# Kernel tuning notes

Hardware: AMD Instinct MI355X
Metric: run time of the kernel (lower is better)

The kernel has to match this reference:

```python
import jax, jax.numpy as jnp
from jax import lax
import numpy as np

H, W, C = 128, 128, 1024          # backbone feature map (stride-16, ResNet C4)
STRIDE = 16
NUM_ANCHORS = 9                   # 3 scales x 3 ratios
IOU_THRESHOLD = 0.7
SCORE_THRESHOLD = 0.5


def _make_anchors():
    scales = np.array([128.0, 256.0, 512.0], np.float32)
    ratios = np.array([0.5, 1.0, 2.0], np.float32)
    hs = (scales[:, None] * np.sqrt(ratios)[None, :]).reshape(-1)   # [9]
    ws = (scales[:, None] / np.sqrt(ratios)[None, :]).reshape(-1)   # [9]
    cy = (np.arange(H, dtype=np.float32) + 0.5) * STRIDE
    cx = (np.arange(W, dtype=np.float32) + 0.5) * STRIDE
    anc = np.zeros((H, W, NUM_ANCHORS, 4), np.float32)
    anc[..., 0] = cy[:, None, None]
    anc[..., 1] = cx[None, :, None]
    anc[..., 2] = hs
    anc[..., 3] = ws
    return anc.reshape(-1, 4)      # [N,4] as (cy, cx, h, w)


def _conv(x, w, b):
    return lax.conv_general_dilated(
        x, w, (1, 1), 'SAME', dimension_numbers=('NHWC', 'HWIO', 'NHWC')) + b


def _rpn_head(features, w1, b1, w2, b2, w_score, b_score, w_box, b_box):
    x = jax.nn.relu(features)
    x = _conv(x, w1, b1)
    x = jax.nn.relu(x)
    x = _conv(x, w2, b2)
    scores = jax.nn.sigmoid(_conv(x, w_score, b_score))   # [1,H,W,9]
    shifts = _conv(x, w_box, b_box)                        # [1,H,W,36]
    return scores.reshape(-1, 1), shifts.reshape(-1, 4)


def _decode(shifts, anchors):
    acy, acx, ah, aw = anchors[:, 0], anchors[:, 1], anchors[:, 2], anchors[:, 3]
    dy, dx, dh, dw = shifts[:, 0], shifts[:, 1], shifts[:, 2], shifts[:, 3]
    cy = acy + dy * ah
    cx = acx + dx * aw
    h = ah * jnp.exp(dh)
    w = aw * jnp.exp(dw)
    y1 = jnp.clip(cy - 0.5 * h, 0.0, H * STRIDE)
    x1 = jnp.clip(cx - 0.5 * w, 0.0, W * STRIDE)
    y2 = jnp.clip(cy + 0.5 * h, 0.0, H * STRIDE)
    x2 = jnp.clip(cx + 0.5 * w, 0.0, W * STRIDE)
    return jnp.stack([y1, x1, y2, x2], axis=-1)            # [N,4]


def _nms(boxes, scores, max_out):
    """Greedy NMS like tf.image.non_max_suppression, fixed-size padded output."""
    n = boxes.shape[0]
    areas = (boxes[:, 2] - boxes[:, 0]) * (boxes[:, 3] - boxes[:, 1])

    def body(state):
        suppressed, sel, count = state
        masked = jnp.where(suppressed, -jnp.inf, scores)
        i = jnp.argmax(masked)
        valid = masked[i] >= SCORE_THRESHOLD
        sel = sel.at[count].set(jnp.where(valid, i.astype(jnp.int32), -1))
        count = count + valid.astype(jnp.int32)
        b = boxes[i]
        iy = jnp.maximum(0.0, jnp.minimum(b[2], boxes[:, 2]) - jnp.maximum(b[0], boxes[:, 0]))
        ix = jnp.maximum(0.0, jnp.minimum(b[3], boxes[:, 3]) - jnp.maximum(b[1], boxes[:, 1]))
        inter = iy * ix
        iou = inter / (areas[i] + areas - inter + 1e-9)
        new_sup = (suppressed | (iou > IOU_THRESHOLD)).at[i].set(True)
        suppressed = jnp.where(valid, new_sup, jnp.ones_like(suppressed))
        return suppressed, sel, count

    def cond(state):
        suppressed, sel, count = state
        return (count < max_out) & (~jnp.all(suppressed))

    sel0 = jnp.full((max_out,), -1, jnp.int32)
    sup0 = jnp.zeros((n,), bool)
    _, sel, _ = lax.while_loop(cond, body, (sup0, sel0, jnp.int32(0)))
    valid = sel >= 0
    idx = jnp.where(valid, sel, 0)
    return boxes[idx] * valid[:, None], scores[idx] * valid, valid


def setup_inputs() -> dict:
    key = jax.random.key(0)
    ks = jax.random.split(key, 5)
    def init_w(k, shape, fan_in, scale=1.0):
        return jax.random.normal(k, shape, jnp.float32) * (scale / np.sqrt(fan_in))
    features = jax.random.normal(ks[0], (1, H, W, C), jnp.float32)
    w1 = init_w(ks[1], (3, 3, C, 512), 9 * C)
    b1 = jnp.zeros((512,), jnp.float32)
    w2 = init_w(ks[2], (3, 3, 512, 512), 9 * 512)
    b2 = jnp.zeros((512,), jnp.float32)
    w_score = init_w(ks[3], (1, 1, 512, NUM_ANCHORS), 512)
    b_score = jnp.zeros((NUM_ANCHORS,), jnp.float32)
    w_box = init_w(ks[4], (1, 1, 512, 4 * NUM_ANCHORS), 512, scale=0.1)
    b_box = jnp.zeros((4 * NUM_ANCHORS,), jnp.float32)
    return {"features": features, "w1": w1, "b1": b1, "w2": w2, "b2": b2,
            "w_score": w_score, "b_score": b_score,
            "w_box": w_box, "b_box": b_box, "region_limit": 300}


def reference(features, w1, b1, w2, b2, w_score, b_score, w_box, b_box, region_limit):
    pred_scores, pred_shifts = _rpn_head(features, w1, b1, w2, b2,
                                         w_score, b_score, w_box, b_box)
    anchors = jnp.asarray(_make_anchors())
    boxes = _decode(pred_shifts, anchors)
    return _nms(boxes, pred_scores[:, 0], int(region_limit))
```

## Files before the change

### kernel.cpp

```cpp
#include <hip/hip_runtime.h>

#define HW 128
#define COUTC 512
#define NB 4097
#define NSEL 300
#define T_TOP 4096
#define TW 64
#define FAST_N 1024

typedef _Float16 half8 __attribute__((ext_vector_type(8)));
typedef _Float16 half4v __attribute__((ext_vector_type(4)));
typedef float floatx4 __attribute__((ext_vector_type(4)));

#define NWS_A1H   ((size_t)0)
#define NWS_A1L   ((size_t)34611200)
#define NWS_W1H   ((size_t)69222400)
#define NWS_W1L   ((size_t)78659584)
#define NWS_A2H   ((size_t)88096768)
#define NWS_A2L   ((size_t)105402368)
#define NWS_W2H   ((size_t)122707968)
#define NWS_W2L   ((size_t)127426560)
#define NWS_X2    ((size_t)132145152)
#define NWS_BOXES ((size_t)165699584)
#define NWS_KEYS  ((size_t)168058880)
#define NWS_SKEYS ((size_t)169238528)
#define NWS_HIST  ((size_t)170418176)
#define NWS_CUR   ((size_t)170434816)
#define NWS_CNT   ((size_t)170451456)
#define NWS_BASE  ((size_t)170451712)
#define NWS_TOTAL ((size_t)170468352)

#define WS_X1     ((size_t)0)
#define WS_X2     ((size_t)33554432)
#define WS_BOXES  ((size_t)67108864)
#define WS_KEYS   ((size_t)69468160)
#define WS_SKEYS  ((size_t)70647808)
#define WS_HIST   ((size_t)71827456)
#define WS_CUR    ((size_t)71844096)
#define WS_CNT    ((size_t)71860736)
#define WS_BASE   ((size_t)71860992)

__device__ __forceinline__ void glds16(const void* g, void* l) {
    __builtin_amdgcn_global_load_lds(
        (const __attribute__((address_space(1))) void*)g,
        (__attribute__((address_space(3))) void*)l, 16, 0, 0);
}


__global__ __launch_bounds__(256) void convert_feat_kernel(
    const float* __restrict__ feat, _Float16* __restrict__ ah, _Float16* __restrict__ al)
{
    __shared__ __align__(16) _Float16 lh[130 * 32];
    __shared__ __align__(16) _Float16 ll[130 * 32];
    int pr = blockIdx.x;
    int chunk = blockIdx.y;
    int t = threadIdx.x;
    int c  = t & 31;
    int pg = t >> 5;
    bool interior = (pr >= 1 && pr <= 128);
    if (interior) {
        for (int px = pg; px < 128; px += 8) {
            float x = feat[((size_t)(pr - 1) * 128 + px) * 1024 + chunk * 32 + c];
            x = fmaxf(x, 0.f);
            _Float16 hi = (_Float16)x;
            lh[(px + 1) * 32 + c] = hi;
            ll[(px + 1) * 32 + c] = (_Float16)(x - (float)hi);
        }
    } else {
        for (int px = pg; px < 128; px += 8) {
            lh[(px + 1) * 32 + c] = (_Float16)0.f;
            ll[(px + 1) * 32 + c] = (_Float16)0.f;
        }
    }
    if (t < 32) {
        lh[t] = (_Float16)0.f;          ll[t] = (_Float16)0.f;
        lh[129 * 32 + t] = (_Float16)0.f; ll[129 * 32 + t] = (_Float16)0.f;
    }
    __syncthreads();
    size_t base = (size_t)pr * 133120 + (size_t)chunk * 4160;
    for (int i = t; i < 520; i += 256) {
        int sub = i / 130;
        int pc  = i - sub * 130;
        *(float4*)&ah[base + sub * 1040 + pc * 8] = *(const float4*)&lh[pc * 32 + sub * 8];
        *(float4*)&al[base + sub * 1040 + pc * 8] = *(const float4*)&ll[pc * 32 + sub * 8];
    }
}

template<int CIN>
__device__ __forceinline__ void convert_w_body(
    int b, const float* __restrict__ w, _Float16* __restrict__ wh, _Float16* __restrict__ wl)
{
    constexpr int NU = CIN / 8;
    int gid = b * 256 + threadIdx.x;
    int oc = gid & 511;
    int rest = gid >> 9;
    int u = rest & (NU - 1);
    int tap = rest / NU;
    if (tap >= 9) return;
    int k0 = u * 8;
    half8 vh, vl;
    #pragma unroll
    for (int j = 0; j < 8; ++j) {
        float v = w[((size_t)tap * CIN + k0 + j) * 512 + oc] * 64.f;
        _Float16 hi = (_Float16)v;
        vh[j] = hi;
        vl[j] = (_Float16)(v - (float)hi);
    }
    size_t o = (size_t)tap * CIN * 512 + (size_t)(k0 >> 5) * 16384
             + (size_t)((k0 >> 3) & 3) * 4096 + (size_t)oc * 8;
    *(half8*)(wh + o) = vh;
    *(half8*)(wl + o) = vl;
}

__global__ __launch_bounds__(256) void prep_kernel(
    const float* __restrict__ w1, _Float16* __restrict__ w1h, _Float16* __restrict__ w1l,
    const float* __restrict__ w2, _Float16* __restrict__ w2h, _Float16* __restrict__ w2l,
    const float* __restrict__ w_s, const float* __restrict__ w_b,
    _Float16* __restrict__ wbh, _Float16* __restrict__ wbl,
    _Float16* __restrict__ a2h, _Float16* __restrict__ a2l)
{
    int b = blockIdx.x;
    if (b < 2304) { convert_w_body<1024>(b, w1, w1h, w1l); return; }
    if (b < 3456) { convert_w_body<512>(b - 2304, w2, w2h, w2l); return; }
    if (b < 3584) {
        int gid = (b - 3456) * 256 + threadIdx.x;
        int n = gid & 63;
        int k = gid >> 6;
        float v = 0.f;
        if (n < 9)       v = w_s[k * 9 + n] * 64.f;
        else if (n < 45) v = w_b[k * 36 + (n - 9)] * 64.f;
        _Float16 hi = (_Float16)v;
        size_t o = (size_t)(k >> 5) * 2048 + (size_t)((k >> 3) & 3) * 512 + (size_t)n * 8 + (k & 7);
        wbh[o] = hi;
        wbl[o] = (_Float16)(v - (float)hi);
        return;
    }
    {
        int i = b - 3584;
        int pr, pc;
        if (i < 130)      { pr = 0;        pc = i; }
        else if (i < 260) { pr = 129;      pc = i - 130; }
        else if (i < 388) { pr = i - 259;  pc = 0; }
        else              { pr = i - 387;  pc = 129; }
        int t = threadIdx.x;
        if (t >= 128) return;
        _Float16* dst = (t & 64) ? a2l : a2h;
        int u = t & 63;
        size_t o = (size_t)pr * 66560 + (size_t)(u >> 2) * 4160 + (size_t)(u & 3) * 1040 + (size_t)pc * 8;
        *(float4*)(dst + o) = make_float4(0.f, 0.f, 0.f, 0.f);
    }
}

template<int CIN, bool PAD>
__global__ __launch_bounds__(256) void conv_mfma_kernel(
    const _Float16* __restrict__ ah, const _Float16* __restrict__ al,
    const _Float16* __restrict__ wh, const _Float16* __restrict__ wl,
    const float* __restrict__ bias,
    _Float16* __restrict__ oh, _Float16* __restrict__ ol)
{
    constexpr int ROWSTR = CIN * 130;
    constexpr int TAPW   = CIN * 512;
    __shared__ __align__(16) _Float16 lds[32768];

    int b  = blockIdx.x;
    int bx = ((b & 7) << 6) | (b >> 3);
    int h  = bx & 127;
    int n0 = (bx >> 7) << 7;

    int tid  = threadIdx.x;
    int wave = tid >> 6;
    int lane = tid & 63;
    int fr = lane & 15;
    int fq = lane >> 4;

    int aoff0 = fq * 1040 + (32 * wave + fr) * 8;
    int aoff1 = aoff0 + 128;
    int boff0 = fq * 4096 + (n0 + 32 * wave + fr) * 8;
    int boff1 = boff0 + 128;

    int wm = wave & 1, wn = wave >> 1;

    floatx4 acc[4][4];
    #pragma unroll
    for (int i = 0; i < 4; ++i)
        #pragma unroll
        for (int j = 0; j < 4; ++j)
            acc[i][j] = (floatx4){0.f, 0.f, 0.f, 0.f};

    #pragma unroll
    for (int tap = 0; tap < 9; ++tap) {
        int dy = tap / 3 - 1, dx = tap % 3 - 1;
        const _Float16* gAh = ah + (size_t)(h + dy + 1) * ROWSTR + (dx + 1) * 8;
        const _Float16* gAl = al + (size_t)(h + dy + 1) * ROWSTR + (dx + 1) * 8;
        const _Float16* gBh = wh + (size_t)tap * TAPW;
        const _Float16* gBl = wl + (size_t)tap * TAPW;

        for (int kc = 0; kc < CIN; kc += 64) {
            #pragma unroll
            for (int s = 0; s < 2; ++s) {
                int ab = ((kc >> 5) + s) * 4160;
                int bb = ((kc >> 5) + s) * 16384;
                _Float16* A0 = lds +          s * 4096 + 2 * wave * 512;
                _Float16* L0 = lds + 8192  +  s * 4096 + 2 * wave * 512;
                _Float16* B0 = lds + 16384 +  s * 4096 + 2 * wave * 512;
                _Float16* C0 = lds + 24576 +  s * 4096 + 2 * wave * 512;
                glds16(gAh + ab + aoff0, A0);
                glds16(gAh + ab + aoff1, A0 + 512);
                glds16(gAl + ab + aoff0, L0);
                glds16(gAl + ab + aoff1, L0 + 512);
                glds16(gBh + bb + boff0, B0);
                glds16(gBh + bb + boff1, B0 + 512);
                glds16(gBl + bb + boff0, C0);
                glds16(gBl + bb + boff1, C0 + 512);
            }
            __syncthreads();

            #pragma unroll
            for (int s = 0; s < 2; ++s) {
                const _Float16* rAh = lds +          s * 4096 + wm * 2048 + fq * 128 + fr * 8;
                const _Float16* rAl = rAh + 8192;
                const _Float16* rBh = lds + 16384 +  s * 4096 + wn * 2048 + fq * 128 + fr * 8;
                const _Float16* rBl = rBh + 8192;

                half8 fah[4], fal[4], fbh[4], fbl[4];
                #pragma unroll
                for (int i = 0; i < 4; ++i) {
                    fah[i] = *(const half8*)(rAh + i * 512);
                    fal[i] = *(const half8*)(rAl + i * 512);
                    fbh[i] = *(const half8*)(rBh + i * 512);
                    fbl[i] = *(const half8*)(rBl + i * 512);
                }
                #pragma unroll
                for (int i = 0; i < 4; ++i)
                    #pragma unroll
                    for (int j = 0; j < 4; ++j)
                        acc[i][j] = __builtin_amdgcn_mfma_f32_16x16x32_f16(fah[i], fbh[j], acc[i][j], 0, 0, 0);
                #pragma unroll
                for (int i = 0; i < 4; ++i)
                    #pragma unroll
                    for (int j = 0; j < 4; ++j)
                        acc[i][j] = __builtin_amdgcn_mfma_f32_16x16x32_f16(fah[i], fbl[j], acc[i][j], 0, 0, 0);
                #pragma unroll
                for (int i = 0; i < 4; ++i)
                    #pragma unroll
                    for (int j = 0; j < 4; ++j)
                        acc[i][j] = __builtin_amdgcn_mfma_f32_16x16x32_f16(fal[i], fbh[j], acc[i][j], 0, 0, 0);
            }
            __syncthreads();
        }
    }

    const float scale = 1.f / 64.f;
    int em = 64 * wm + fq * 4;
    int en = 64 * wn + fr;
    #pragma unroll
    for (int j = 0; j < 4; ++j) {
        int oc = n0 + en + 16 * j;
        float b2 = bias[oc];
        #pragma unroll
        for (int i = 0; i < 4; ++i) {
            #pragma unroll
            for (int r = 0; r < 4; ++r) {
                int w = em + 16 * i + r;
                float v = fmaf(acc[i][j][r], scale, b2);
                if (PAD) {
                    v = fmaxf(v, 0.f);
                    _Float16 hi = (_Float16)v;
                    size_t o = (size_t)(h + 1) * 66560 + (size_t)(oc >> 5) * 4160
                             + (size_t)((oc >> 3) & 3) * 1040 + (size_t)(w + 1) * 8 + (oc & 7);
                    oh[o] = hi;
                    ol[o] = (_Float16)(v - (float)hi);
                } else {
                    _Float16 hi = (_Float16)v;
                    size_t o = (size_t)h * 65536 + (size_t)(oc >> 5) * 4096
                             + (size_t)((oc >> 3) & 3) * 1024 + (size_t)w * 8 + (oc & 7);
                    oh[o] = hi;
                    ol[o] = (_Float16)(v - (float)hi);
                }
            }
        }
    }
}

__device__ __forceinline__ void decode_emit(
    int gi, float z, float dyv, float dxv, float dhv, float dwv,
    float4* __restrict__ boxes, unsigned long long* __restrict__ keys,
    int* __restrict__ cnt, int* __restrict__ hist)
{
    int a = gi % 9;
    int pix = gi / 9;
    int h = pix >> 7, w = pix & 127;
    float sc  = (a < 3) ? 128.f : ((a < 6) ? 256.f : 512.f);
    int r = a - (a / 3) * 3;
    float ratio = (r == 0) ? 0.5f : ((r == 1) ? 1.f : 2.f);
    float sr = sqrtf(ratio);
    float ahh = sc * sr, aww = sc / sr;
    float acy = ((float)h + 0.5f) * 16.f;
    float acx = ((float)w + 0.5f) * 16.f;
    float cy = fmaf(dyv, ahh, acy);
    float cx = fmaf(dxv, aww, acx);
    float hh = ahh * expf(dhv);
    float ww = aww * expf(dwv);
    float y1 = fminf(fmaxf(cy - 0.5f * hh, 0.f), 2048.f);
    float x1 = fminf(fmaxf(cx - 0.5f * ww, 0.f), 2048.f);
    float y2 = fminf(fmaxf(cy + 0.5f * hh, 0.f), 2048.f);
    float x2 = fminf(fmaxf(cx + 0.5f * ww, 0.f), 2048.f);
    boxes[gi] = make_float4(y1, x1, y2, x2);
    float s = 1.f / (1.f + expf(-z));
    if (s >= 0.5f) {
        unsigned u = __float_as_uint(s);
        unsigned d = 0x3F800000u - u;
        unsigned long long key = ((unsigned long long)d << 18) | (unsigned)gi;
        int p = atomicAdd(cnt, 1);
        keys[p] = key;
        atomicAdd(&hist[d >> 11], 1);
    }
}

__global__ __launch_bounds__(256) void heads_mfma_kernel(
    const _Float16* __restrict__ xh, const _Float16* __restrict__ xl,
    const _Float16* __restrict__ wbh, const _Float16* __restrict__ wbl,
    const float* __restrict__ b_s, const float* __restrict__ b_b,
    float4* __restrict__ boxes, unsigned long long* __restrict__ keys,
    int* __restrict__ cnt, int* __restrict__ hist)
{
    __shared__ __align__(16) char smem[24576];
    _Float16* sAh = (_Float16*)smem;
    _Float16* sAl = (_Float16*)(smem + 8192);
    _Float16* sBh = (_Float16*)(smem + 16384);
    _Float16* sBl = (_Float16*)(smem + 20480);
    float* outs = (float*)smem;
    __shared__ float sb[48];

    int tid  = threadIdx.x;
    int wave = tid >> 6;
    int lane = tid & 63;
    int fr = lane & 15;
    int fq = lane >> 4;
    if (tid < 48) sb[tid] = (tid < 9) ? b_s[tid] : ((tid < 45) ? b_b[tid - 9] : 0.f);

    int h = blockIdx.x;
    int wm = wave & 1, wn = wave >> 1;

    floatx4 acc[4][2];
    #pragma unroll
    for (int i = 0; i < 4; ++i)
        #pragma unroll
        for (int j = 0; j < 2; ++j)
            acc[i][j] = (floatx4){0.f, 0.f, 0.f, 0.f};

    for (int kc = 0; kc < 16; ++kc) {
        const _Float16* gxh = xh + (size_t)h * 65536 + kc * 4096;
        const _Float16* gxl = xl + (size_t)h * 65536 + kc * 4096;
        glds16(gxh + tid * 8,        sAh + tid * 8);
        glds16(gxh + 2048 + tid * 8, sAh + 2048 + tid * 8);
        glds16(gxl + tid * 8,        sAl + tid * 8);
        glds16(gxl + 2048 + tid * 8, sAl + 2048 + tid * 8);
        glds16(wbh + kc * 2048 + tid * 8, sBh + tid * 8);
        glds16(wbl + kc * 2048 + tid * 8, sBl + tid * 8);
        __syncthreads();

        half8 fah[4], fal[4], fbh[2], fbl[2];
        #pragma unroll
        for (int i = 0; i < 4; ++i) {
            int px = wm * 64 + 16 * i + fr;
            int aaddr = fq * 1024 + px * 8;
            fah[i] = *(const half8*)(sAh + aaddr);
            fal[i] = *(const half8*)(sAl + aaddr);
        }
        #pragma unroll
        for (int j = 0; j < 2; ++j) {
            int n = wn * 32 + 16 * j + fr;
            int baddr = fq * 512 + n * 8;
            fbh[j] = *(const half8*)(sBh + baddr);
            fbl[j] = *(const half8*)(sBl + baddr);
        }
        #pragma unroll
        for (int i = 0; i < 4; ++i)
            #pragma unroll
            for (int j = 0; j < 2; ++j) {
                acc[i][j] = __builtin_amdgcn_mfma_f32_16x16x32_f16(fah[i], fbh[j], acc[i][j], 0, 0, 0);
                acc[i][j] = __builtin_amdgcn_mfma_f32_16x16x32_f16(fah[i], fbl[j], acc[i][j], 0, 0, 0);
                acc[i][j] = __builtin_amdgcn_mfma_f32_16x16x32_f16(fal[i], fbh[j], acc[i][j], 0, 0, 0);
            }
        __syncthreads();
    }

    const float scale = 1.f / 64.f;
    #pragma unroll
    for (int i = 0; i < 4; ++i)
        #pragma unroll
        for (int j = 0; j < 2; ++j)
            #pragma unroll
            for (int r = 0; r < 4; ++r) {
                int px = wm * 64 + 16 * i + fq * 4 + r;
                int n = wn * 32 + 16 * j + fr;
                if (n < 48)
                    outs[px * 48 + n] = fmaf(acc[i][j][r], scale, sb[n]);
            }
    __syncthreads();

    if (tid < 128) {
        int p = tid;
        #pragma unroll
        for (int a = 0; a < 9; ++a) {
            float z   = outs[p * 48 + a];
            float dyv = outs[p * 48 + 9 + 4 * a + 0];
            float dxv = outs[p * 48 + 9 + 4 * a + 1];
            float dhv = outs[p * 48 + 9 + 4 * a + 2];
            float dwv = outs[p * 48 + 9 + 4 * a + 3];
            int gi = (h * 128 + p) * 9 + a;
            decode_emit(gi, z, dyv, dxv, dhv, dwv, boxes, keys, cnt, hist);
        }
    }
}

template<int CIN, bool RELU_IN, bool RELU_OUT>
__global__ __launch_bounds__(256) void conv3x3_kernel(
    const float* __restrict__ in, const float* __restrict__ wgt,
    const float* __restrict__ bias, float* __restrict__ out)
{
    __shared__ float As[32][68];
    __shared__ float Bs[32][64];
    int bx = blockIdx.x;
    int mtile = bx & 255, ntile = bx >> 8;
    int h = mtile >> 1, w0 = (mtile & 1) << 6, n0 = ntile << 6;
    int tid = threadIdx.x, ty = tid >> 4, tx = tid & 15;
    float acc[4][4] = {{0.f}};
    const int KTOT = 9 * CIN;
    for (int k0 = 0; k0 < KTOT; k0 += 32) {
        int tap = k0 / CIN, icb = k0 % CIN;
        int dy = tap / 3 - 1, dx = tap % 3 - 1;
        int row = h + dy;
        bool rowok = ((unsigned)row < HW);
        {
            int pix = tid >> 3, cs = (tid & 7) << 2;
            #pragma unroll
            for (int p = 0; p < 2; ++p) {
                int px = pix + p * 32;
                int wcol = w0 + px + dx;
                float4 v = make_float4(0.f, 0.f, 0.f, 0.f);
                if (rowok && (unsigned)wcol < HW) {
                    v = *(const float4*)&in[((size_t)row * HW + wcol) * CIN + icb + cs];
                    if (RELU_IN) {
                        v.x = fmaxf(v.x, 0.f); v.y = fmaxf(v.y, 0.f);
                        v.z = fmaxf(v.z, 0.f); v.w = fmaxf(v.w, 0.f);
                    }
                }
                As[cs + 0][px] = v.x; As[cs + 1][px] = v.y;
                As[cs + 2][px] = v.z; As[cs + 3][px] = v.w;
            }
        }
        {
            int kr = tid >> 4, nc = (tid & 15) << 2;
            #pragma unroll
            for (int p = 0; p < 2; ++p) {
                int k = kr + p * 16;
                *(float4*)&Bs[k][nc] = *(const float4*)&wgt[(size_t)(k0 + k) * COUTC + n0 + nc];
            }
        }
        __syncthreads();
        #pragma unroll
        for (int kk = 0; kk < 32; ++kk) {
            float4 a = *(const float4*)&As[kk][ty << 2];
            float4 b = *(const float4*)&Bs[kk][tx << 2];
            float av[4] = {a.x, a.y, a.z, a.w};
            float bv[4] = {b.x, b.y, b.z, b.w};
            #pragma unroll
            for (int i = 0; i < 4; ++i)
                #pragma unroll
                for (int j = 0; j < 4; ++j)
                    acc[i][j] = fmaf(av[i], bv[j], acc[i][j]);
        }
        __syncthreads();
    }
    float4 bi = *(const float4*)&bias[n0 + (tx << 2)];
    float bv2[4] = {bi.x, bi.y, bi.z, bi.w};
    #pragma unroll
    for (int i = 0; i < 4; ++i) {
        float4 o;
        o.x = acc[i][0] + bv2[0]; o.y = acc[i][1] + bv2[1];
        o.z = acc[i][2] + bv2[2]; o.w = acc[i][3] + bv2[3];
        if (RELU_OUT) {
            o.x = fmaxf(o.x, 0.f); o.y = fmaxf(o.y, 0.f);
            o.z = fmaxf(o.z, 0.f); o.w = fmaxf(o.w, 0.f);
        }
        *(float4*)&out[((size_t)(h * HW) + w0 + (ty << 2) + i) * COUTC + n0 + (tx << 2)] = o;
    }
}

__global__ __launch_bounds__(256) void heads_decode_kernel(
    const float* __restrict__ x, const float* __restrict__ w_s, const float* __restrict__ b_s,
    const float* __restrict__ w_b, const float* __restrict__ b_b,
    float4* __restrict__ boxes, unsigned long long* __restrict__ keys,
    int* __restrict__ cnt, int* __restrict__ hist)
{
    __shared__ float xs[4][512];
    __shared__ float outs[4][45];
    int wave = threadIdx.x >> 6;
    int lane = threadIdx.x & 63;
    int pix  = blockIdx.x * 4 + wave;

    const float4* xp = (const float4*)&x[(size_t)pix * COUTC];
    *(float4*)&xs[wave][lane * 4]       = xp[lane];
    *(float4*)&xs[wave][256 + lane * 4] = xp[64 + lane];
    __syncthreads();

    if (lane < 45) {
        const float* wp; int stride; float acc;
        if (lane < 9) { wp = w_s + lane;       stride = 9;  acc = b_s[lane]; }
        else          { wp = w_b + (lane - 9); stride = 36; acc = b_b[lane - 9]; }
        const float* xrow = xs[wave];
        for (int k = 0; k < 512; k += 4) {
            acc = fmaf(xrow[k + 0], wp[(k + 0) * stride], acc);
            acc = fmaf(xrow[k + 1], wp[(k + 1) * stride], acc);
            acc = fmaf(xrow[k + 2], wp[(k + 2) * stride], acc);
            acc = fmaf(xrow[k + 3], wp[(k + 3) * stride], acc);
        }
        outs[wave][lane] = acc;
    }
    __syncthreads();

    if (lane < 9) {
        int a = lane;
        decode_emit(pix * 9 + a, outs[wave][a],
                    outs[wave][9 + 4 * a + 0], outs[wave][9 + 4 * a + 1],
                    outs[wave][9 + 4 * a + 2], outs[wave][9 + 4 * a + 3],
                    boxes, keys, cnt, hist);
    }
}

__global__ __launch_bounds__(256) void scan_kernel(
    const int* __restrict__ hist, int* __restrict__ base)
{
    __shared__ int tot[256];
    int t = threadIdx.x;
    int v[16];
    int s = 0;
    #pragma unroll
    for (int i = 0; i < 16; ++i) { v[i] = hist[t * 16 + i]; s += v[i]; }
    tot[t] = s;
    __syncthreads();
    for (int d = 1; d < 256; d <<= 1) {
        int x = (t >= d) ? tot[t - d] : 0;
        __syncthreads();
        tot[t] += x;
        __syncthreads();
    }
    int excl = (t == 0) ? 0 : tot[t - 1];
    #pragma unroll
    for (int i = 0; i < 16; ++i) { base[t * 16 + i] = excl; excl += v[i]; }
    if (t == 255) { base[4096] = excl; base[4097] = excl + hist[4096]; }
}

__global__ __launch_bounds__(256) void scatter_kernel(
    const unsigned long long* __restrict__ keys, const int* __restrict__ cnt,
    const int* __restrict__ base, int* __restrict__ cur,
    unsigned long long* __restrict__ skeys)
{
    int i = blockIdx.x * 256 + threadIdx.x;
    if (i < *cnt) {
        unsigned long long k = keys[i];
        int b = (int)(k >> 29);
        int p = base[b] + atomicAdd(&cur[b], 1);
        skeys[p] = k;
    }
}

__global__ __launch_bounds__(256) void sortb_kernel(
    const unsigned long long* __restrict__ skeys, const int* __restrict__ base,
    const float4* __restrict__ boxes,
    unsigned long long* __restrict__ sk2,
    float4* __restrict__ cboxes, float* __restrict__ careas)
{
    __shared__ unsigned long long sk[2048];
    int b = blockIdx.x;
    int s0 = base[b];
    int n = base[b + 1] - s0;
    if (n <= 0) return;
    int t = threadIdx.x;
    if (n <= 2048) {
        for (int i = t; i < n; i += 256) sk[i] = skeys[s0 + i];
        __syncthreads();
        for (int i = t; i < n; i += 256) {
            unsigned long long k = sk[i];
            int r = 0;
            for (int j = 0; j < n; ++j) r += (sk[j] < k) ? 1 : 0;
            int pos = s0 + r;
            sk2[pos] = k;
            if (pos < T_TOP) {
                float4 bb = boxes[k & 0x3FFFFull];
                cboxes[pos] = bb;
                careas[pos] = (bb.z - bb.x) * (bb.w - bb.y);
            }
        }
    } else {
        const unsigned long long* src = skeys + s0;
        for (int i = t; i < n; i += 256) {
            unsigned long long k = src[i];
            int r = 0;
            for (int j = 0; j < n; ++j) r += (src[j] < k) ? 1 : 0;
            int pos = s0 + r;
            sk2[pos] = k;
            if (pos < T_TOP) {
                float4 bb = boxes[k & 0x3FFFFull];
                cboxes[pos] = bb;
                careas[pos] = (bb.z - bb.x) * (bb.w - bb.y);
            }
        }
    }
}

__global__ __launch_bounds__(256) void mask_kernel(
    const float4* __restrict__ cboxes, const float* __restrict__ careas,
    unsigned long long* __restrict__ msk)
{
    int bi = blockIdx.y, bj = blockIdx.x;
    if (bj < bi) return;
    __shared__ float4 jb[256];
    __shared__ float  ja[256];
    int t = threadIdx.x;
    int j0 = bj << 8;
    jb[t] = cboxes[j0 + t];
    ja[t] = careas[j0 + t];
    __syncthreads();
    int i = (bi << 8) + t;
    float4 ci = cboxes[i];
    float ca = careas[i];
    unsigned long long word = 0;
    for (int jj = 0; jj < 256; ++jj) {
        int j = j0 + jj;
        float4 b = jb[jj];
        float iy = fmaxf(0.f, fminf(ci.z, b.z) - fmaxf(ci.x, b.x));
        float ix = fmaxf(0.f, fminf(ci.w, b.w) - fmaxf(ci.y, b.y));
        float inter = iy * ix;
        float iou = inter / (ca + ja[jj] - inter + 1e-9f);
        bool bit = (j == i) || (j > i && iou > 0.7f);
        if (bit) word |= 1ull << (jj & 63);
        if ((jj & 63) == 63) {
            msk[(size_t)i * TW + (bj << 2) + (jj >> 6)] = word;
            word = 0;
        }
    }
}

__global__ __launch_bounds__(256) void walk_kernel(
    const unsigned long long* __restrict__ sk2, const int* __restrict__ cnt,
    const float4* __restrict__ cboxes, const float* __restrict__ careas,
    const unsigned long long* __restrict__ msk, const float4* __restrict__ boxes,
    float* __restrict__ out)
{
    __shared__ unsigned long long mlds[FAST_N * 16];
    __shared__ unsigned long long sup[TW];
    __shared__ float4 sbox[NSEL];
    __shared__ float  sarea[NSEL];
    __shared__ unsigned short sellist[NSEL];
    int tid = threadIdx.x;
    for (int i = tid; i < 1800; i += 256) out[i] = 0.f;
    int total = *cnt;
    int Tc = min(total, T_TOP);
    int FN = min(Tc, FAST_N);
    for (int i = tid; i < FN * 16; i += 256) {
        mlds[i] = msk[(size_t)(i >> 4) * TW + (i & 15)];
    }
    if (tid < TW) sup[tid] = 0ull;
    __syncthreads();
    if (tid >= 64) return;
    int lane = tid;
    int sel = 0;

    {
        int p = 0;
        while (sel < NSEL) {
            int w0 = p >> 6;
            unsigned long long m = 0;
            if (lane < 16 && lane >= w0) {
                m = ~sup[lane];
                if (lane == w0) m &= (~0ull << (p & 63));
            }
            unsigned long long bal = __ballot(m != 0ull);
            if (bal == 0ull) break;
            int w = __builtin_ctzll(bal);
            int bit = __shfl(m ? __builtin_ctzll(m) : 0, w);
            int c = (w << 6) + bit;
            if (c >= FN) break;
            float4 cb = cboxes[c];
            float ca = careas[c];
            if (lane == 0) {
                unsigned long long key = sk2[c];
                out[sel * 4 + 0] = cb.x; out[sel * 4 + 1] = cb.y;
                out[sel * 4 + 2] = cb.z; out[sel * 4 + 3] = cb.w;
                out[1200 + sel] = __uint_as_float(0x3F800000u - (unsigned)(key >> 18));
                out[1500 + sel] = 1.f;
                sbox[sel] = cb;
                sarea[sel] = ca;
                sellist[sel] = (unsigned short)c;
            }
            sel++;
            if (lane < 16) sup[lane] |= mlds[c * 16 + lane];
            p = c + 1;
        }
    }

    if (sel < NSEL && Tc > FN) {
        unsigned long long acc = 0ull;
        if (lane >= 16) {
            for (int s = 0; s < sel; ++s)
                acc |= msk[(size_t)sellist[s] * TW + lane];
            sup[lane] = acc;
        }

        auto scanFrom = [&](int p) -> int {
            if (p < 0 || p >= Tc) return -1;
            int w = p >> 6;
            unsigned long long f = (~sup[w]) & (~0ull << (p & 63));
            while (f == 0ull) {
                ++w;
                if (w >= TW) return -1;
                f = ~sup[w];
            }
            int c = (w << 6) + __builtin_ctzll(f);
            return (c < Tc) ? c : -1;
        };

        unsigned long long r0 = 0, r1 = 0, r2n = 0;
        int idx = scanFrom(FN);
        if (idx >= 0) r0 = msk[(size_t)idx * TW + lane];
        int idx2 = (idx >= 0) ? scanFrom(idx + 1) : -1;
        if (idx2 >= 0) r1 = msk[(size_t)idx2 * TW + lane];

        while (idx >= 0 && sel < NSEL) {
            float4 cb = cboxes[idx];
            float ca = careas[idx];
            if (lane == 0) {
                unsigned long long key = sk2[idx];
                out[sel * 4 + 0] = cb.x; out[sel * 4 + 1] = cb.y;
                out[sel * 4 + 2] = cb.z; out[sel * 4 + 3] = cb.w;
                out[1200 + sel] = __uint_as_float(0x3F800000u - (unsigned)(key >> 18));
                out[1500 + sel] = 1.f;
                sbox[sel] = cb;
                sarea[sel] = ca;
            }
            sel++;
            if (sel >= NSEL) break;

            int idx3 = (idx2 >= 0) ? scanFrom(idx2 + 1) : -1;
            if (idx3 >= 0) r2n = msk[(size_t)idx3 * TW + lane];

            sup[lane] |= r0;

            if (idx2 >= 0) {
                unsigned long long w = sup[idx2 >> 6];
                if ((w >> (idx2 & 63)) & 1ull) {
                    idx2 = scanFrom(idx2);
                    if (idx2 >= 0) r1 = msk[(size_t)idx2 * TW + lane];
                    idx3 = (idx2 >= 0) ? scanFrom(idx2 + 1) : -1;
                    if (idx3 >= 0) r2n = msk[(size_t)idx3 * TW + lane];
                }
            }
            idx = idx2; r0 = r1;
            idx2 = idx3; r1 = r2n;
        }
    }

    if (sel < NSEL && total > T_TOP) {
        for (int i = T_TOP; i < total && sel < NSEL; ++i) {
            unsigned long long key = sk2[i];
            float4 cb = boxes[key & 0x3FFFFull];
            float ca = (cb.z - cb.x) * (cb.w - cb.y);
            int supp = 0;
            for (int t = lane; t < sel; t += 64) {
                float4 s4 = sbox[t];
                float iy = fmaxf(0.f, fminf(s4.z, cb.z) - fmaxf(s4.x, cb.x));
                float ix = fmaxf(0.f, fminf(s4.w, cb.w) - fmaxf(s4.y, cb.y));
                float inter = iy * ix;
                float iou = inter / (sarea[t] + ca - inter + 1e-9f);
                if (iou > 0.7f) supp = 1;
            }
            if (__ballot(supp) == 0ull) {
                if (lane == 0) {
                    out[sel * 4 + 0] = cb.x; out[sel * 4 + 1] = cb.y;
                    out[sel * 4 + 2] = cb.z; out[sel * 4 + 3] = cb.w;
                    out[1200 + sel] = __uint_as_float(0x3F800000u - (unsigned)(key >> 18));
                    out[1500 + sel] = 1.f;
                    sbox[sel] = cb;
                    sarea[sel] = ca;
                }
                sel++;
            }
        }
    }
}

extern "C" void kernel_launch(void* const* d_in, const int* in_sizes, int n_in,
                              void* d_out, int out_size, void* d_ws, size_t ws_size,
                              hipStream_t stream) {
    const float* feat = (const float*)d_in[0];
    const float* w1   = (const float*)d_in[1];
    const float* b1   = (const float*)d_in[2];
    const float* w2   = (const float*)d_in[3];
    const float* b2   = (const float*)d_in[4];
    const float* w_s  = (const float*)d_in[5];
    const float* b_s  = (const float*)d_in[6];
    const float* w_b  = (const float*)d_in[7];
    const float* b_b  = (const float*)d_in[8];
    float* out = (float*)d_out;
    char* ws = (char*)d_ws;

    if (ws_size >= NWS_TOTAL) {
        _Float16* a1h = (_Float16*)(ws + NWS_A1H);
        _Float16* a1l = (_Float16*)(ws + NWS_A1L);
        _Float16* w1h = (_Float16*)(ws + NWS_W1H);
        _Float16* w1l = (_Float16*)(ws + NWS_W1L);
        _Float16* a2h = (_Float16*)(ws + NWS_A2H);
        _Float16* a2l = (_Float16*)(ws + NWS_A2L);
        _Float16* w2h = (_Float16*)(ws + NWS_W2H);
        _Float16* w2l = (_Float16*)(ws + NWS_W2L);
        _Float16* xh  = (_Float16*)(ws + NWS_X2);
        _Float16* xl  = (_Float16*)(ws + NWS_X2 + 16777216);
        float4* boxes = (float4*)(ws + NWS_BOXES);
        unsigned long long* keys  = (unsigned long long*)(ws + NWS_KEYS);
        unsigned long long* skeys = (unsigned long long*)(ws + NWS_SKEYS);
        int* hist = (int*)(ws + NWS_HIST);
        int* cur  = (int*)(ws + NWS_CUR);
        int* cnt  = (int*)(ws + NWS_CNT);
        int* base = (int*)(ws + NWS_BASE);
        _Float16* wbh = (_Float16*)(ws + NWS_SKEYS);
        _Float16* wbl = (_Float16*)(ws + NWS_SKEYS + 65536);
        unsigned long long* msk = (unsigned long long*)(ws + NWS_A1H);
        float4* cbox  = (float4*)(ws + NWS_A1L);
        float*  carea = (float*)(ws + NWS_A1L + 262144);
        unsigned long long* sk2 = keys;

        hipMemsetAsync(ws + NWS_HIST, 0, (NWS_CNT - NWS_HIST) + 256, stream);
        convert_feat_kernel<<<dim3(130, 32), 256, 0, stream>>>(feat, a1h, a1l);
        prep_kernel<<<4100, 256, 0, stream>>>(w1, w1h, w1l, w2, w2h, w2l,
                                              w_s, w_b, wbh, wbl, a2h, a2l);
        conv_mfma_kernel<1024, true ><<<512, 256, 0, stream>>>(a1h, a1l, w1h, w1l, b1, a2h, a2l);
        conv_mfma_kernel< 512, false><<<512, 256, 0, stream>>>(a2h, a2l, w2h, w2l, b2, xh, xl);
        heads_mfma_kernel<<<128, 256, 0, stream>>>(xh, xl, wbh, wbl, b_s, b_b, boxes, keys, cnt, hist);
        scan_kernel<<<1, 256, 0, stream>>>(hist, base);
        scatter_kernel<<<576, 256, 0, stream>>>(keys, cnt, base, cur, skeys);
        sortb_kernel<<<NB, 256, 0, stream>>>(skeys, base, boxes, sk2, cbox, carea);
        mask_kernel<<<dim3(16, 16), 256, 0, stream>>>(cbox, carea, msk);
        walk_kernel<<<1, 256, 0, stream>>>(sk2, cnt, cbox, carea, msk, boxes, out);
    } else {
        float* x1 = (float*)(ws + WS_X1);
        float* x2 = (float*)(ws + WS_X2);
        float4* boxes = (float4*)(ws + WS_BOXES);
        unsigned long long* keys  = (unsigned long long*)(ws + WS_KEYS);
        unsigned long long* skeys = (unsigned long long*)(ws + WS_SKEYS);
        int* hist = (int*)(ws + WS_HIST);
        int* cur  = (int*)(ws + WS_CUR);
        int* cnt  = (int*)(ws + WS_CNT);
        int* base = (int*)(ws + WS_BASE);
        unsigned long long* msk = (unsigned long long*)(ws + WS_X1);
        float4* cbox  = (float4*)(ws + WS_X2);
        float*  carea = (float*)(ws + WS_X2 + 262144);
        unsigned long long* sk2 = keys;

        hipMemsetAsync(ws + WS_HIST, 0, (WS_CNT - WS_HIST) + 256, stream);
        conv3x3_kernel<1024, true,  true ><<<2048, 256, 0, stream>>>(feat, w1, b1, x1);
        conv3x3_kernel< 512, false, false><<<2048, 256, 0, stream>>>(x1,   w2, b2, x2);
        heads_decode_kernel<<<4096, 256, 0, stream>>>(x2, w_s, b_s, w_b, b_b, boxes, keys, cnt, hist);
        scan_kernel<<<1, 256, 0, stream>>>(hist, base);
        scatter_kernel<<<576, 256, 0, stream>>>(keys, cnt, base, cur, skeys);
        sortb_kernel<<<NB, 256, 0, stream>>>(skeys, base, boxes, sk2, cbox, carea);
        mask_kernel<<<dim3(16, 16), 256, 0, stream>>>(cbox, carea, msk);
        walk_kernel<<<1, 256, 0, stream>>>(sk2, cnt, cbox, carea, msk, boxes, out);
    }
}
```

Measured before the change: 944.2 us.

## Halve conv output-channel tile and K chunk to double block count

The conv MFMA kernel now covers 64 output channels per block instead of 128 and walks K in 32-wide steps instead of 64. This doubles the grid to 1024 blocks, shrinks LDS from 64KB to 24KB, and halves the accumulator registers, aiming for higher occupancy and better load balance across CUs. The XCD-aware block swizzle is removed. In exchange, each activation tile is loaded twice as often (lower A reuse) and there are twice as many barriers per FLOP.

```diff
diff --git a/kernel.cpp b/kernel.cpp
--- a/kernel.cpp
+++ b/kernel.cpp
@@ -160,12 +160,11 @@
 {
     constexpr int ROWSTR = CIN * 130;
     constexpr int TAPW   = CIN * 512;
-    __shared__ __align__(16) _Float16 lds[32768];
-
-    int b  = blockIdx.x;
-    int bx = ((b & 7) << 6) | (b >> 3);
+    __shared__ __align__(16) _Float16 lds[12288];
+
+    int bx = blockIdx.x;
     int h  = bx & 127;
-    int n0 = (bx >> 7) << 7;
+    int n0 = (bx >> 7) << 6;
 
     int tid  = threadIdx.x;
     int wave = tid >> 6;
@@ -175,17 +174,26 @@
 
     int aoff0 = fq * 1040 + (32 * wave + fr) * 8;
     int aoff1 = aoff0 + 128;
-    int boff0 = fq * 4096 + (n0 + 32 * wave + fr) * 8;
-    int boff1 = boff0 + 128;
+    int boffB = fq * 4096 + (n0 + 32 * (wave & 1) + 16 * (wave >> 1) + fr) * 8;
 
     int wm = wave & 1, wn = wave >> 1;
 
-    floatx4 acc[4][4];
+    floatx4 acc[4][2];
     #pragma unroll
     for (int i = 0; i < 4; ++i)
         #pragma unroll
-        for (int j = 0; j < 4; ++j)
+        for (int j = 0; j < 2; ++j)
             acc[i][j] = (floatx4){0.f, 0.f, 0.f, 0.f};
+
+    _Float16* A0 = lds + wave * 1024;
+    _Float16* L0 = lds + 4096 + wave * 1024;
+    _Float16* B0 = lds + 8192 + (wave & 1) * 1024 + (wave >> 1) * 512;
+    _Float16* C0 = B0 + 2048;
+
+    const _Float16* rAh = lds + wm * 2048 + fq * 128 + fr * 8;
+    const _Float16* rAl = rAh + 4096;
+    const _Float16* rBh = lds + 8192 + wn * 1024 + fq * 128 + fr * 8;
+    const _Float16* rBl = rBh + 2048;
 
     #pragma unroll
     for (int tap = 0; tap < 9; ++tap) {
@@ -195,66 +203,52 @@
         const _Float16* gBh = wh + (size_t)tap * TAPW;
         const _Float16* gBl = wl + (size_t)tap * TAPW;
 
-        for (int kc = 0; kc < CIN; kc += 64) {
-            #pragma unroll
-            for (int s = 0; s < 2; ++s) {
-                int ab = ((kc >> 5) + s) * 4160;
-                int bb = ((kc >> 5) + s) * 16384;
-                _Float16* A0 = lds +          s * 4096 + 2 * wave * 512;
-                _Float16* L0 = lds + 8192  +  s * 4096 + 2 * wave * 512;
-                _Float16* B0 = lds + 16384 +  s * 4096 + 2 * wave * 512;
-                _Float16* C0 = lds + 24576 +  s * 4096 + 2 * wave * 512;
-                glds16(gAh + ab + aoff0, A0);
-                glds16(gAh + ab + aoff1, A0 + 512);
-                glds16(gAl + ab + aoff0, L0);
-                glds16(gAl + ab + aoff1, L0 + 512);
-                glds16(gBh + bb + boff0, B0);
-                glds16(gBh + bb + boff1, B0 + 512);
-                glds16(gBl + bb + boff0, C0);
-                glds16(gBl + bb + boff1, C0 + 512);
-            }
+        for (int kc = 0; kc < CIN; kc += 32) {
+            int ab = (kc >> 5) * 4160;
+            int bb = (kc >> 5) * 16384;
+            glds16(gAh + ab + aoff0, A0);
+            glds16(gAh + ab + aoff1, A0 + 512);
+            glds16(gAl + ab + aoff0, L0);
+            glds16(gAl + ab + aoff1, L0 + 512);
+            glds16(gBh + bb + boffB, B0);
+            glds16(gBl + bb + boffB, C0);
             __syncthreads();
 
-            #pragma unroll
-            for (int s = 0; s < 2; ++s) {
-                const _Float16* rAh = lds +          s * 4096 + wm * 2048 + fq * 128 + fr * 8;
-                const _Float16* rAl = rAh + 8192;
-                const _Float16* rBh = lds + 16384 +  s * 4096 + wn * 2048 + fq * 128 + fr * 8;
-                const _Float16* rBl = rBh + 8192;
-
-                half8 fah[4], fal[4], fbh[4], fbl[4];
+            half8 fah[4], fal[4], fbh[2], fbl[2];
+            #pragma unroll
+            for (int i = 0; i < 4; ++i) {
+                fah[i] = *(const half8*)(rAh + i * 512);
+                fal[i] = *(const half8*)(rAl + i * 512);
+            }
+            #pragma unroll
+            for (int j = 0; j < 2; ++j) {
+                fbh[j] = *(const half8*)(rBh + j * 512);
+                fbl[j] = *(const half8*)(rBl + j * 512);
+            }
+            #pragma unroll
+            for (int i = 0; i < 4; ++i)
                 #pragma unroll
-                for (int i = 0; i < 4; ++i) {
-                    fah[i] = *(const half8*)(rAh + i * 512);
-                    fal[i] = *(const half8*)(rAl + i * 512);
-                    fbh[i] = *(const half8*)(rBh + i * 512);
-                    fbl[i] = *(const half8*)(rBl + i * 512);
-                }
+                for (int j = 0; j < 2; ++j)
+                    acc[i][j] = __builtin_amdgcn_mfma_f32_16x16x32_f16(fah[i], fbh[j], acc[i][j], 0, 0, 0);
+            #pragma unroll
+            for (int i = 0; i < 4; ++i)
                 #pragma unroll
-                for (int i = 0; i < 4; ++i)
-                    #pragma unroll
-                    for (int j = 0; j < 4; ++j)
-                        acc[i][j] = __builtin_amdgcn_mfma_f32_16x16x32_f16(fah[i], fbh[j], acc[i][j], 0, 0, 0);
+                for (int j = 0; j < 2; ++j)
+                    acc[i][j] = __builtin_amdgcn_mfma_f32_16x16x32_f16(fah[i], fbl[j], acc[i][j], 0, 0, 0);
+            #pragma unroll
+            for (int i = 0; i < 4; ++i)
                 #pragma unroll
-                for (int i = 0; i < 4; ++i)
-                    #pragma unroll
-                    for (int j = 0; j < 4; ++j)
-                        acc[i][j] = __builtin_amdgcn_mfma_f32_16x16x32_f16(fah[i], fbl[j], acc[i][j], 0, 0, 0);
-                #pragma unroll
-                for (int i = 0; i < 4; ++i)
-                    #pragma unroll
-                    for (int j = 0; j < 4; ++j)
-                        acc[i][j] = __builtin_amdgcn_mfma_f32_16x16x32_f16(fal[i], fbh[j], acc[i][j], 0, 0, 0);
-            }
+                for (int j = 0; j < 2; ++j)
+                    acc[i][j] = __builtin_amdgcn_mfma_f32_16x16x32_f16(fal[i], fbh[j], acc[i][j], 0, 0, 0);
             __syncthreads();
         }
     }
 
     const float scale = 1.f / 64.f;
     int em = 64 * wm + fq * 4;
-    int en = 64 * wn + fr;
+    int en = 32 * wn + fr;
     #pragma unroll
-    for (int j = 0; j < 4; ++j) {
+    for (int j = 0; j < 2; ++j) {
         int oc = n0 + en + 16 * j;
         float b2 = bias[oc];
         #pragma unroll
@@ -836,8 +830,8 @@
         convert_feat_kernel<<<dim3(130, 32), 256, 0, stream>>>(feat, a1h, a1l);
         prep_kernel<<<4100, 256, 0, stream>>>(w1, w1h, w1l, w2, w2h, w2l,
                                               w_s, w_b, wbh, wbl, a2h, a2l);
-        conv_mfma_kernel<1024, true ><<<512, 256, 0, stream>>>(a1h, a1l, w1h, w1l, b1, a2h, a2l);
-        conv_mfma_kernel< 512, false><<<512, 256, 0, stream>>>(a2h, a2l, w2h, w2l, b2, xh, xl);
+        conv_mfma_kernel<1024, true ><<<1024, 256, 0, stream>>>(a1h, a1l, w1h, w1l, b1, a2h, a2l);
+        conv_mfma_kernel< 512, false><<<1024, 256, 0, stream>>>(a2h, a2l, w2h, w2l, b2, xh, xl);
         heads_mfma_kernel<<<128, 256, 0, stream>>>(xh, xl, wbh, wbl, b_s, b_b, boxes, keys, cnt, hist);
         scan_kernel<<<1, 256, 0, stream>>>(hist, base);
         scatter_kernel<<<576, 256, 0, stream>>>(keys, cnt, base, cur, skeys);
```

Measured after the change: 998.7 us. +5.8%, slower.
